# Kernel optimization log

Measured on AMD Instinct MI355X. Metric: run time of the kernel, lower is better.

## Reference

```python
import jax, jax.numpy as jnp
import numpy as np

N = 20000      # nodes
E = 320000     # edges
C = 8          # n_species (input 0e multiplicity)
H = 128        # hidden multiplicity per irrep
RB = 8         # radial basis size
RM = 64        # radial mlp width
CUTOFF = 5.0
P = 2.0        # polynomial cutoff power
AVG_N = 16.0   # avg_n_neighbors
SQRT3 = float(np.sqrt(3.0))


def _w(k, i, o, scale=1.0):
    return jax.random.normal(k, (i, o), jnp.float32) * np.sqrt(scale / i)


def setup_inputs() -> dict:
    key = jax.random.key(0)
    ks = jax.random.split(key, 24)
    return {
        'displacements': jax.random.normal(ks[0], (E, 3), jnp.float32) * 1.5,
        'species': jax.random.randint(ks[1], (N,), 0, C, dtype=jnp.int32),
        'senders': jax.random.randint(ks[2], (E,), 0, N, dtype=jnp.int32),
        'receivers': jax.random.randint(ks[3], (E,), 0, N, dtype=jnp.int32),
        'l1_lin1': _w(ks[4], C, C),
        'l1_rw0': _w(ks[5], RB, RM, 4.0),
        'l1_rw1': _w(ks[6], RM, RM, 4.0),
        'l1_rw2': _w(ks[7], RM, RM, 4.0),
        'l1_rw3': _w(ks[8], RM, 2 * C),
        'l1_w2s': _w(ks[9], C, 2 * H),
        'l1_w2v': _w(ks[10], C, H),
        'l1_skip': jax.random.normal(ks[11], (C, C, 2 * H), jnp.float32) / np.sqrt(C),
        'l2_lin1s': _w(ks[12], H, H),
        'l2_lin1v': _w(ks[13], H, H),
        'l2_rw0': _w(ks[14], RB, RM, 4.0),
        'l2_rw1': _w(ks[15], RM, RM, 4.0),
        'l2_rw2': _w(ks[16], RM, RM, 4.0),
        'l2_rw3': _w(ks[17], RM, 2 * H),
        'l2_w2': _w(ks[18], 2 * H, H),
        'l2_skip': jax.random.normal(ks[19], (C, H, H), jnp.float32) / np.sqrt(H),
        'readout_w': _w(ks[20], H, 1),
    }


def _bessel(x):
    w = jnp.linspace(1.0, RB, RB) * jnp.pi
    xs = x[:, None]
    safe = jnp.where(xs == 0.0, 1.0, xs)
    return (2.0 / CUTOFF) * jnp.where(xs == 0.0, w / CUTOFF, jnp.sin(w * xs / CUTOFF) / safe)


def _poly_cutoff(x):
    u = x / CUTOFF
    out = 1.0 - (P + 1.0) * (P + 2.0) / 2.0 * u ** P \
        + P * (P + 2.0) * u ** (P + 1.0) \
        - P * (P + 1.0) / 2.0 * u ** (P + 2.0)
    return out * jnp.where(u < 1.0, 1.0, 0.0)


def _radial(rb, w0, w1, w2, w3):
    h = jax.nn.silu(rb @ w0)
    h = jax.nn.silu(h @ w1)
    h = jax.nn.silu(h @ w2)
    return h @ w3


def _node_energies(displacements, species, senders, receivers,
                   l1_lin1, l1_rw0, l1_rw1, l1_rw2, l1_rw3, l1_w2s, l1_w2v, l1_skip,
                   l2_lin1s, l2_lin1v, l2_rw0, l2_rw1, l2_rw2, l2_rw3, l2_w2, l2_skip,
                   readout_w):
    sq = jnp.sum(displacements ** 2, axis=-1)
    rn = jnp.where(sq == 0.0, 0.0, jnp.sqrt(jnp.where(sq == 0.0, 1.0, sq)))
    rb = _bessel(rn) * _poly_cutoff(rn)[:, None]                     # (E,RB)
    unit = displacements / jnp.where(rn == 0.0, 1.0, rn)[:, None]
    Y1 = SQRT3 * unit                                                # 1o SH, component norm
    onehot = jax.nn.one_hot(species, C, dtype=displacements.dtype)   # (N,C) = Cx0e features
    inv_sqrt_nbr = 1.0 / np.sqrt(AVG_N)

    # ---- layer 1: Cx0e -> 128x0e + 128x1o ----
    s = (onehot @ l1_lin1)[senders]                                  # (E,C)
    R = _radial(rb, l1_rw0, l1_rw1, l1_rw2, l1_rw3)                  # (E,2C)
    msg_s = s * R[:, :C]                                             # 0e x 0e -> 0e
    msg_v = s[:, :, None] * Y1[:, None, :] * R[:, C:, None]          # 0e x 1o -> 1o (E,C,3)
    agg_s = jax.ops.segment_sum(msg_s, receivers, num_segments=N) * inv_sqrt_nbr
    agg_v = jax.ops.segment_sum(msg_v, receivers, num_segments=N) * inv_sqrt_nbr
    scal = agg_s @ l1_w2s + jnp.einsum('nc,ncd->nd', onehot, l1_skip[species])  # (N,2H)
    vec = jnp.einsum('nci,cd->ndi', agg_v, l1_w2v)                   # (N,H,3)
    # gate: first H even scalars -> silu, last H scalars gate the 1o vectors
    x0 = jax.nn.silu(scal[:, :H])
    x1 = vec * jax.nn.silu(scal[:, H:])[:, :, None]

    # ---- layer 2: 128x0e + 128x1o -> 128x0e ----
    s2 = (x0 @ l2_lin1s)[senders]                                    # (E,H)
    v2 = jnp.einsum('nci,cd->ndi', x1, l2_lin1v)[senders]            # (E,H,3)
    tp = jnp.concatenate([s2, jnp.einsum('eci,ei->ec', v2, Y1) / SQRT3], axis=-1)  # (E,2H)
    R2 = _radial(rb, l2_rw0, l2_rw1, l2_rw2, l2_rw3)                 # (E,2H)
    agg2 = jax.ops.segment_sum(tp * R2, receivers, num_segments=N) * inv_sqrt_nbr
    feat = jax.nn.silu(agg2 @ l2_w2 + jnp.einsum('nc,ncd->nd', x0, l2_skip[species]))

    return feat @ readout_w                                          # (N,1) node energies


def reference(displacements, l1_lin1, l1_rw0, l1_rw1, l1_rw2, l1_rw3, l1_w2s, l1_w2v,
              l1_skip, l2_lin1s, l2_lin1v, l2_rw0, l2_rw1, l2_rw2, l2_rw3, l2_w2,
              l2_skip, readout_w, species, senders, receivers):
    return _node_energies(displacements, species, senders, receivers,
                          l1_lin1, l1_rw0, l1_rw1, l1_rw2, l1_rw3, l1_w2s, l1_w2v, l1_skip,
                          l2_lin1s, l2_lin1v, l2_rw0, l2_rw1, l2_rw2, l2_rw3, l2_w2, l2_skip,
                          readout_w)
```

## Files before the change

kernel.cpp:

```cpp
#include <hip/hip_runtime.h>
#include <math.h>

#define NN_ 20000
#define EE_ 320000

__device__ __forceinline__ float silu_f(float x) { return x / (1.0f + expf(-x)); }

template<int IN, int OUT, bool ACT>
__device__ __forceinline__ void dense(const float* __restrict__ W,
                                      const float* __restrict__ in,
                                      float* __restrict__ out) {
  float acc[OUT];
#pragma unroll
  for (int j = 0; j < OUT; ++j) acc[j] = 0.f;
#pragma unroll
  for (int k = 0; k < IN; ++k) {
    const float x = in[k];
#pragma unroll
    for (int j = 0; j < OUT; ++j) acc[j] = fmaf(x, W[k * OUT + j], acc[j]);
  }
#pragma unroll
  for (int j = 0; j < OUT; ++j) out[j] = ACT ? silu_f(acc[j]) : acc[j];
}

__global__ __launch_bounds__(256) void k_hist(const int* __restrict__ receivers,
                                              int* __restrict__ hist) {
  const int e = blockIdx.x * 256 + threadIdx.x;
  atomicAdd(&hist[receivers[e]], 1);
}

__global__ __launch_bounds__(1024) void k_scan(const int* __restrict__ hist,
                                               int* __restrict__ offs,
                                               int* __restrict__ cursor) {
  __shared__ int lds[1024];
  __shared__ int carry_s;
  const int t = threadIdx.x;
  if (t == 0) carry_s = 0;
  __syncthreads();
  for (int base = 0; base < NN_; base += 1024) {
    const int i = base + t;
    const int v = (i < NN_) ? hist[i] : 0;
    lds[t] = v;
    __syncthreads();
    for (int d = 1; d < 1024; d <<= 1) {
      const int tv = (t >= d) ? lds[t - d] : 0;
      __syncthreads();
      lds[t] += tv;
      __syncthreads();
    }
    const int inc = lds[t];
    const int c = carry_s;
    if (i < NN_) {
      const int off = c + inc - v;
      offs[i] = off;
      cursor[i] = off;
    }
    __syncthreads();
    if (t == 0) carry_s = c + lds[1023];
    __syncthreads();
  }
  if (t == 0) offs[NN_] = carry_s;
}

__global__ __launch_bounds__(256) void k_scatter(const int* __restrict__ receivers,
                                                 int* __restrict__ cursor,
                                                 int* __restrict__ edge_id) {
  const int e = blockIdx.x * 256 + threadIdx.x;
  const int r = receivers[e];
  const int pos = atomicAdd(&cursor[r], 1);
  edge_id[pos] = e;
}

__global__ __launch_bounds__(256) void k1a_edge(
    const float* __restrict__ disp, const int* __restrict__ species,
    const int* __restrict__ senders,
    const float* __restrict__ lin1,
    const float* __restrict__ rw0, const float* __restrict__ rw1,
    const float* __restrict__ rw2, const float* __restrict__ rw3,
    float* __restrict__ buf1, float* __restrict__ rbc_g, float* __restrict__ y1_g) {
  const int e = blockIdx.x * 256 + threadIdx.x;
  const float dx = disp[e * 3 + 0], dy = disp[e * 3 + 1], dz = disp[e * 3 + 2];
  const float sq = dx * dx + dy * dy + dz * dz;
  const float rn = sqrtf(sq);
  const float inv = (rn == 0.f) ? 1.f : (1.f / rn);
  const float u = rn * 0.2f;
  float fc;
  {
    const float u2 = u * u;
    fc = 1.f - 6.f * u2 + 8.f * u2 * u - 3.f * u2 * u2;
    fc = (u < 1.f) ? fc : 0.f;
  }
  float rb[8];
#pragma unroll
  for (int k = 0; k < 8; ++k) {
    const float wk = (float)(k + 1) * 3.14159265358979323846f;
    const float s = (rn == 0.f) ? (wk * 0.2f) : (sinf(wk * u) * inv);
    rb[k] = 0.4f * s * fc;
  }
  float4 r0 = {rb[0], rb[1], rb[2], rb[3]};
  float4 r1 = {rb[4], rb[5], rb[6], rb[7]};
  *(float4*)(rbc_g + e * 8) = r0;
  *(float4*)(rbc_g + e * 8 + 4) = r1;
  const float y1x = 1.7320508075688772f * dx * inv;
  const float y1y = 1.7320508075688772f * dy * inv;
  const float y1z = 1.7320508075688772f * dz * inv;
  float4 y4 = {y1x, y1y, y1z, 0.f};
  *(float4*)(y1_g + e * 4) = y4;

  float h0[64], h1[64], R[16];
  dense<8, 64, true>(rw0, rb, h0);
  dense<64, 64, true>(rw1, h0, h1);
  dense<64, 64, true>(rw2, h1, h0);
  dense<64, 16, false>(rw3, h0, R);

  const int sp = species[senders[e]];
  float m[32];
#pragma unroll
  for (int c = 0; c < 8; ++c) {
    const float sc = lin1[sp * 8 + c];
    m[c] = sc * R[c];
    const float mv = sc * R[8 + c];
    m[8 + c * 3 + 0] = mv * y1x;
    m[8 + c * 3 + 1] = mv * y1y;
    m[8 + c * 3 + 2] = mv * y1z;
  }
  float* dst = buf1 + (size_t)e * 32;
#pragma unroll
  for (int q = 0; q < 8; ++q) {
    float4 v = {m[q * 4 + 0], m[q * 4 + 1], m[q * 4 + 2], m[q * 4 + 3]};
    *(float4*)(dst + q * 4) = v;
  }
}

__global__ __launch_bounds__(256) void k1b_gather(
    const float* __restrict__ buf1, const int* __restrict__ offs,
    const int* __restrict__ edge_id,
    float* __restrict__ agg_s, float* __restrict__ agg_v) {
  const int n = blockIdx.x * 8 + (threadIdx.x >> 5);
  const int ch = threadIdx.x & 31;
  const int beg = offs[n], end = offs[n + 1];
  float acc = 0.f;
  for (int i = beg; i < end; ++i) {
    const int eid = edge_id[i];
    acc += buf1[(size_t)eid * 32 + ch];
  }
  if (ch < 8) agg_s[n * 8 + ch] = acc;
  else agg_v[n * 24 + (ch - 8)] = acc;
}

__global__ __launch_bounds__(64) void k2a_node(
    const float* __restrict__ agg_s, const float* __restrict__ agg_v,
    const int* __restrict__ species,
    const float* __restrict__ w2s, const float* __restrict__ w2v,
    const float* __restrict__ skip1,
    float* __restrict__ x0_g, float* __restrict__ x1_g) {
  const int n = blockIdx.x;
  const int l = threadIdx.x;
  __shared__ float g_lds[128];
  const int sp = species[n];
  float as[8];
#pragma unroll
  for (int k = 0; k < 8; ++k) as[k] = agg_s[n * 8 + k] * 0.25f;
  float sc[4];
#pragma unroll
  for (int j = 0; j < 4; ++j) {
    const int d = l * 4 + j;
    float a = skip1[(sp * 9) * 256 + d];
#pragma unroll
    for (int k = 0; k < 8; ++k) a = fmaf(as[k], w2s[k * 256 + d], a);
    sc[j] = silu_f(a);
  }
  if (l < 32) {
#pragma unroll
    for (int j = 0; j < 4; ++j) x0_g[n * 128 + l * 4 + j] = sc[j];
  } else {
#pragma unroll
    for (int j = 0; j < 4; ++j) g_lds[(l - 32) * 4 + j] = sc[j];
  }
  __syncthreads();
  float av[24];
#pragma unroll
  for (int k = 0; k < 24; ++k) av[k] = agg_v[n * 24 + k] * 0.25f;
#pragma unroll
  for (int h = 0; h < 2; ++h) {
    const int d = l + h * 64;
    const float g = g_lds[d];
    float v0 = 0.f, v1 = 0.f, v2v = 0.f;
#pragma unroll
    for (int c = 0; c < 8; ++c) {
      const float w = w2v[c * 128 + d];
      v0 = fmaf(av[c * 3 + 0], w, v0);
      v1 = fmaf(av[c * 3 + 1], w, v1);
      v2v = fmaf(av[c * 3 + 2], w, v2v);
    }
    x1_g[(n * 3 + 0) * 128 + d] = v0 * g;
    x1_g[(n * 3 + 1) * 128 + d] = v1 * g;
    x1_g[(n * 3 + 2) * 128 + d] = v2v * g;
  }
}

__global__ __launch_bounds__(256) void k2b_gemm(
    const float* __restrict__ x0_g, const float* __restrict__ x1_g,
    const int* __restrict__ species,
    const float* __restrict__ lin1s, const float* __restrict__ lin1v,
    const float* __restrict__ skip2,
    float* __restrict__ s2_g, float* __restrict__ v2_g,
    float* __restrict__ skipv_g) {
  const int w = __builtin_amdgcn_readfirstlane((int)(threadIdx.x >> 6));
  const int l = threadIdx.x & 63;
  const int nbase = blockIdx.x * 32 + w * 8;
  float s2a[8] = {}, s2b[8] = {}, ska[8] = {}, skb[8] = {};
  float v2a[8][3] = {}, v2b[8][3] = {};
  int sp[8];
#pragma unroll
  for (int nn = 0; nn < 8; ++nn) sp[nn] = species[nbase + nn];
  for (int c = 0; c < 128; ++c) {
    const float wA0 = lin1s[c * 128 + l];
    const float wA1 = lin1s[c * 128 + 64 + l];
    const float wB0 = lin1v[c * 128 + l];
    const float wB1 = lin1v[c * 128 + 64 + l];
#pragma unroll
    for (int nn = 0; nn < 8; ++nn) {
      const int n = nbase + nn;
      const float x0v = x0_g[n * 128 + c];
      const float wS0 = skip2[sp[nn] * 16384 + c * 128 + l];
      const float wS1 = skip2[sp[nn] * 16384 + c * 128 + 64 + l];
      s2a[nn] = fmaf(x0v, wA0, s2a[nn]);
      s2b[nn] = fmaf(x0v, wA1, s2b[nn]);
      ska[nn] = fmaf(x0v, wS0, ska[nn]);
      skb[nn] = fmaf(x0v, wS1, skb[nn]);
#pragma unroll
      for (int i = 0; i < 3; ++i) {
        const float x1v = x1_g[(n * 3 + i) * 128 + c];
        v2a[nn][i] = fmaf(x1v, wB0, v2a[nn][i]);
        v2b[nn][i] = fmaf(x1v, wB1, v2b[nn][i]);
      }
    }
  }
#pragma unroll
  for (int nn = 0; nn < 8; ++nn) {
    const int n = nbase + nn;
    s2_g[n * 128 + l] = s2a[nn];
    s2_g[n * 128 + 64 + l] = s2b[nn];
    skipv_g[n * 128 + l] = ska[nn];
    skipv_g[n * 128 + 64 + l] = skb[nn];
#pragma unroll
    for (int i = 0; i < 3; ++i) {
      v2_g[n * 384 + l * 3 + i] = v2a[nn][i];
      v2_g[n * 384 + (64 + l) * 3 + i] = v2b[nn][i];
    }
  }
}

__global__ __launch_bounds__(256) void k3a_edge(
    const float* __restrict__ rbc_g,
    const float* __restrict__ rw0, const float* __restrict__ rw1,
    const float* __restrict__ rw2,
    float* __restrict__ ha_buf) {
  const int e = blockIdx.x * 256 + threadIdx.x;
  float rb[8];
  {
    const float4 a = *(const float4*)(rbc_g + e * 8);
    const float4 b = *(const float4*)(rbc_g + e * 8 + 4);
    rb[0] = a.x; rb[1] = a.y; rb[2] = a.z; rb[3] = a.w;
    rb[4] = b.x; rb[5] = b.y; rb[6] = b.z; rb[7] = b.w;
  }
  float h0[64], h1[64];
  dense<8, 64, true>(rw0, rb, h0);
  dense<64, 64, true>(rw1, h0, h1);
  dense<64, 64, true>(rw2, h1, h0);
  float* dst = ha_buf + (size_t)e * 64;
#pragma unroll
  for (int q = 0; q < 16; ++q) {
    float4 v = {h0[q * 4 + 0], h0[q * 4 + 1], h0[q * 4 + 2], h0[q * 4 + 3]};
    *(float4*)(dst + q * 4) = v;
  }
}

__global__ __launch_bounds__(256) void k3b_gather(
    const float* __restrict__ ha_buf, const float* __restrict__ y1_g,
    const int* __restrict__ senders,
    const int* __restrict__ offs, const int* __restrict__ edge_id,
    const float* __restrict__ rw3,
    const float* __restrict__ s2_g, const float* __restrict__ v2_g,
    float* __restrict__ agg2) {
  const int n = blockIdx.x;
  const int ch = threadIdx.x;
  float w[64];
#pragma unroll
  for (int k = 0; k < 64; ++k) w[k] = rw3[k * 256 + ch];
  const int beg = offs[n], end = offs[n + 1];
  const bool is_s = ch < 128;
  const int c3 = (ch - 128) * 3;
  float acc = 0.f;
  for (int i = beg; i < end; ++i) {
    const int eid = __builtin_amdgcn_readfirstlane(edge_id[i]);
    const int s = __builtin_amdgcn_readfirstlane(senders[eid]);
    const float y1x = y1_g[eid * 4 + 0];
    const float y1y = y1_g[eid * 4 + 1];
    const float y1z = y1_g[eid * 4 + 2];
    float tp;
    if (is_s) {
      tp = s2_g[(size_t)s * 128 + ch];
    } else {
      tp = (v2_g[(size_t)s * 384 + c3 + 0] * y1x +
            v2_g[(size_t)s * 384 + c3 + 1] * y1y +
            v2_g[(size_t)s * 384 + c3 + 2] * y1z) * 0.5773502691896258f;
    }
    const float* ha = ha_buf + (size_t)eid * 64;
    float r0 = 0.f, r1 = 0.f, r2 = 0.f, r3 = 0.f;
#pragma unroll
    for (int k = 0; k < 64; k += 4) {
      r0 = fmaf(ha[k + 0], w[k + 0], r0);
      r1 = fmaf(ha[k + 1], w[k + 1], r1);
      r2 = fmaf(ha[k + 2], w[k + 2], r2);
      r3 = fmaf(ha[k + 3], w[k + 3], r3);
    }
    acc = fmaf(tp, (r0 + r1) + (r2 + r3), acc);
  }
  agg2[(size_t)n * 256 + ch] = acc;
}

__global__ __launch_bounds__(256) void k4_node(
    const float* __restrict__ agg2, const float* __restrict__ skipv,
    const float* __restrict__ w2, const float* __restrict__ readout,
    float* __restrict__ out) {
  __shared__ float tile[64 * 65];
  __shared__ float partial[256];
  const int t = threadIdx.x;
  const int w = __builtin_amdgcn_readfirstlane((int)(threadIdx.x >> 6));
  const int l = t & 63;
  const int n0 = blockIdx.x * 64;
  const int n = n0 + l;
  float acc[32];
#pragma unroll
  for (int j = 0; j < 32; ++j) acc[j] = 0.f;
  for (int ko = 0; ko < 256; ko += 64) {
    __syncthreads();
#pragma unroll
    for (int rep = 0; rep < 16; ++rep) {
      const int lin = rep * 256 + t;
      const int node = lin >> 6, kk = lin & 63;
      const int gn = n0 + node;
      tile[kk * 65 + node] = (gn < NN_) ? agg2[(size_t)gn * 256 + ko + kk] * 0.25f : 0.f;
    }
    __syncthreads();
    for (int kk = 0; kk < 64; ++kk) {
      const float a = tile[kk * 65 + l];
#pragma unroll
      for (int jj = 0; jj < 32; ++jj)
        acc[jj] = fmaf(a, w2[(ko + kk) * 128 + w * 32 + jj], acc[jj]);
    }
  }
  float po = 0.f;
  if (n < NN_) {
#pragma unroll
    for (int jj = 0; jj < 32; ++jj) {
      const int d = w * 32 + jj;
      const float v = acc[jj] + skipv[n * 128 + d];
      po = fmaf(silu_f(v), readout[d], po);
    }
  }
  partial[w * 64 + l] = po;
  __syncthreads();
  if (t < 64 && n0 + t < NN_) {
    out[n0 + t] = partial[t] + partial[64 + t] + partial[128 + t] + partial[192 + t];
  }
}

extern "C" void kernel_launch(void* const* d_in, const int* in_sizes, int n_in,
                              void* d_out, int out_size, void* d_ws, size_t ws_size,
                              hipStream_t stream) {
  const float* disp = (const float*)d_in[0];
  const int* species = (const int*)d_in[1];
  const int* senders = (const int*)d_in[2];
  const int* receivers = (const int*)d_in[3];
  const float* l1_lin1 = (const float*)d_in[4];
  const float* l1_rw0 = (const float*)d_in[5];
  const float* l1_rw1 = (const float*)d_in[6];
  const float* l1_rw2 = (const float*)d_in[7];
  const float* l1_rw3 = (const float*)d_in[8];
  const float* l1_w2s = (const float*)d_in[9];
  const float* l1_w2v = (const float*)d_in[10];
  const float* l1_skip = (const float*)d_in[11];
  const float* l2_lin1s = (const float*)d_in[12];
  const float* l2_lin1v = (const float*)d_in[13];
  const float* l2_rw0 = (const float*)d_in[14];
  const float* l2_rw1 = (const float*)d_in[15];
  const float* l2_rw2 = (const float*)d_in[16];
  const float* l2_rw3 = (const float*)d_in[17];
  const float* l2_w2 = (const float*)d_in[18];
  const float* l2_skip = (const float*)d_in[19];
  const float* readout_w = (const float*)d_in[20];

  float* ws = (float*)d_ws;
  float* rbc   = ws;
  float* y1    = ws + 2560000;
  float* s2    = ws + 3840000;
  float* v2    = ws + 6400000;
  float* skipv = ws + 14080000;
  float* agg2  = ws + 16640000;
  float* pool  = ws + 21760000;
  float* agg_s = pool;
  float* agg_v = pool + 160000;
  float* buf1  = pool + 640000;
  float* x0    = pool + 640000;
  float* x1    = pool + 3200000;
  float* ha    = pool;
  int* ibase   = (int*)(ws + 42240000);
  int* hist    = ibase;
  int* cursor  = ibase + 20000;
  int* offs    = ibase + 40000;
  int* edge_id = ibase + 60001;
  if (ws_size < (size_t)(42240000 + 380001) * 4) return;

  hipMemsetAsync(hist, 0, 20000 * sizeof(int), stream);
  k_hist<<<EE_ / 256, 256, 0, stream>>>(receivers, hist);
  k_scan<<<1, 1024, 0, stream>>>(hist, offs, cursor);
  k_scatter<<<EE_ / 256, 256, 0, stream>>>(receivers, cursor, edge_id);

  k1a_edge<<<EE_ / 256, 256, 0, stream>>>(disp, species, senders, l1_lin1,
                                          l1_rw0, l1_rw1, l1_rw2, l1_rw3,
                                          buf1, rbc, y1);
  k1b_gather<<<NN_ / 8, 256, 0, stream>>>(buf1, offs, edge_id, agg_s, agg_v);
  k2a_node<<<NN_, 64, 0, stream>>>(agg_s, agg_v, species, l1_w2s, l1_w2v, l1_skip,
                                   x0, x1);
  k2b_gemm<<<NN_ / 32, 256, 0, stream>>>(x0, x1, species, l2_lin1s, l2_lin1v,
                                         l2_skip, s2, v2, skipv);

  k3a_edge<<<EE_ / 256, 256, 0, stream>>>(rbc, l2_rw0, l2_rw1, l2_rw2, ha);
  k3b_gather<<<NN_, 256, 0, stream>>>(ha, y1, senders, offs, edge_id, l2_rw3,
                                      s2, v2, agg2);
  k4_node<<<(NN_ + 63) / 64, 256, 0, stream>>>(agg2, skipv, l2_w2, readout_w,
                                               (float*)d_out);
}
```

Measured before the change: 1.310 ms.

## Tile radial MLP layers through shared memory with register-blocked 8x8 outer products

The per-edge radial MLP in both layers is changed from one thread per edge holding 64-wide hidden vectors in registers, with weights read from global memory, to a block-cooperative scheme. Each block stages 128 edges' activations and one layer's weights in LDS and computes an 8-edge by 8-output register tile per thread. The aim is to cut register pressure and spilling and to reuse weights across edges. In exchange it adds several block barriers per layer and roughly 50KB of LDS per block, which limits occupancy. The last 64-to-16 layer in layer 1 still reads its weights from global memory per thread.

```diff
diff --git a/kernel.cpp b/kernel.cpp
--- a/kernel.cpp
+++ b/kernel.cpp
@@ -3,24 +3,62 @@
 
 #define NN_ 20000
 #define EE_ 320000
+#define SHP 68
 
 __device__ __forceinline__ float silu_f(float x) { return x / (1.0f + expf(-x)); }
 
-template<int IN, int OUT, bool ACT>
-__device__ __forceinline__ void dense(const float* __restrict__ W,
-                                      const float* __restrict__ in,
-                                      float* __restrict__ out) {
-  float acc[OUT];
-#pragma unroll
-  for (int j = 0; j < OUT; ++j) acc[j] = 0.f;
-#pragma unroll
-  for (int k = 0; k < IN; ++k) {
-    const float x = in[k];
-#pragma unroll
-    for (int j = 0; j < OUT; ++j) acc[j] = fmaf(x, W[k * OUT + j], acc[j]);
-  }
-#pragma unroll
-  for (int j = 0; j < OUT; ++j) out[j] = ACT ? silu_f(acc[j]) : acc[j];
+template<int KD>
+__device__ __forceinline__ void layer_step(float* __restrict__ sh_h,
+                                           const float* __restrict__ sh_w,
+                                           int wavebase, int eg, int jg) {
+  const int jb = jg * 8;
+  float acc[8][8];
+#pragma unroll
+  for (int ee = 0; ee < 8; ++ee)
+#pragma unroll
+    for (int jj = 0; jj < 8; ++jj) acc[ee][jj] = 0.f;
+
+#pragma unroll
+  for (int kc = 0; kc < KD; kc += 4) {
+    float4 w4[4][2];
+#pragma unroll
+    for (int kk = 0; kk < 4; ++kk) {
+      w4[kk][0] = *(const float4*)&sh_w[(kc + kk) * 64 + jb];
+      w4[kk][1] = *(const float4*)&sh_w[(kc + kk) * 64 + jb + 4];
+    }
+    float4 h4[8];
+#pragma unroll
+    for (int ee = 0; ee < 8; ++ee)
+      h4[ee] = *(const float4*)&sh_h[(wavebase + eg + 8 * ee) * SHP + kc];
+#pragma unroll
+    for (int kk = 0; kk < 4; ++kk) {
+#pragma unroll
+      for (int ee = 0; ee < 8; ++ee) {
+        const float hv = ((const float*)&h4[ee])[kk];
+        acc[ee][0] = fmaf(hv, w4[kk][0].x, acc[ee][0]);
+        acc[ee][1] = fmaf(hv, w4[kk][0].y, acc[ee][1]);
+        acc[ee][2] = fmaf(hv, w4[kk][0].z, acc[ee][2]);
+        acc[ee][3] = fmaf(hv, w4[kk][0].w, acc[ee][3]);
+        acc[ee][4] = fmaf(hv, w4[kk][1].x, acc[ee][4]);
+        acc[ee][5] = fmaf(hv, w4[kk][1].y, acc[ee][5]);
+        acc[ee][6] = fmaf(hv, w4[kk][1].z, acc[ee][6]);
+        acc[ee][7] = fmaf(hv, w4[kk][1].w, acc[ee][7]);
+      }
+    }
+  }
+#pragma unroll
+  for (int ee = 0; ee < 8; ++ee) {
+    float* dst = &sh_h[(wavebase + eg + 8 * ee) * SHP + jb];
+    float4 lo = {silu_f(acc[ee][0]), silu_f(acc[ee][1]), silu_f(acc[ee][2]), silu_f(acc[ee][3])};
+    float4 hi = {silu_f(acc[ee][4]), silu_f(acc[ee][5]), silu_f(acc[ee][6]), silu_f(acc[ee][7])};
+    *(float4*)dst = lo;
+    *(float4*)(dst + 4) = hi;
+  }
+}
+
+__device__ __forceinline__ void load_w(const float* __restrict__ W, int nfloat,
+                                       float* __restrict__ dst, int t) {
+  for (int i = t * 4; i < nfloat; i += 512) *(float4*)(dst + i) = *(const float4*)(W + i);
 }
 
 __global__ __launch_bounds__(256) void k_hist(const int* __restrict__ receivers,
@@ -71,14 +109,19 @@
   edge_id[pos] = e;
 }
 
-__global__ __launch_bounds__(256) void k1a_edge(
+__global__ __launch_bounds__(128) void k1a_radial(
     const float* __restrict__ disp, const int* __restrict__ species,
     const int* __restrict__ senders,
     const float* __restrict__ lin1,
     const float* __restrict__ rw0, const float* __restrict__ rw1,
     const float* __restrict__ rw2, const float* __restrict__ rw3,
     float* __restrict__ buf1, float* __restrict__ rbc_g, float* __restrict__ y1_g) {
-  const int e = blockIdx.x * 256 + threadIdx.x;
+  __shared__ float sh_h[128 * SHP];
+  __shared__ float sh_w[64 * 64];
+  const int t = threadIdx.x;
+  const int e0 = blockIdx.x * 128;
+  const int e = e0 + t;
+
   const float dx = disp[e * 3 + 0], dy = disp[e * 3 + 1], dz = disp[e * 3 + 2];
   const float sq = dx * dx + dy * dy + dz * dz;
   const float rn = sqrtf(sq);
@@ -106,12 +149,34 @@
   const float y1z = 1.7320508075688772f * dz * inv;
   float4 y4 = {y1x, y1y, y1z, 0.f};
   *(float4*)(y1_g + e * 4) = y4;
-
-  float h0[64], h1[64], R[16];
-  dense<8, 64, true>(rw0, rb, h0);
-  dense<64, 64, true>(rw1, h0, h1);
-  dense<64, 64, true>(rw2, h1, h0);
-  dense<64, 16, false>(rw3, h0, R);
+  *(float4*)&sh_h[t * SHP] = r0;
+  *(float4*)&sh_h[t * SHP + 4] = r1;
+
+  const int wavebase = (t >> 6) * 64;
+  const int lane = t & 63;
+  const int eg = lane >> 3, jg = lane & 7;
+
+  load_w(rw0, 8 * 64, sh_w, t);
+  __syncthreads();
+  layer_step<8>(sh_h, sh_w, wavebase, eg, jg);
+  __syncthreads();
+  load_w(rw1, 64 * 64, sh_w, t);
+  __syncthreads();
+  layer_step<64>(sh_h, sh_w, wavebase, eg, jg);
+  __syncthreads();
+  load_w(rw2, 64 * 64, sh_w, t);
+  __syncthreads();
+  layer_step<64>(sh_h, sh_w, wavebase, eg, jg);
+  __syncthreads();
+
+  float R[16];
+#pragma unroll
+  for (int c = 0; c < 16; ++c) R[c] = 0.f;
+  for (int k = 0; k < 64; ++k) {
+    const float h = sh_h[t * SHP + k];
+#pragma unroll
+    for (int c = 0; c < 16; ++c) R[c] = fmaf(h, rw3[k * 16 + c], R[c]);
+  }
 
   const int sp = species[senders[e]];
   float m[32];
@@ -129,6 +194,45 @@
   for (int q = 0; q < 8; ++q) {
     float4 v = {m[q * 4 + 0], m[q * 4 + 1], m[q * 4 + 2], m[q * 4 + 3]};
     *(float4*)(dst + q * 4) = v;
+  }
+}
+
+__global__ __launch_bounds__(128) void k3a_radial(
+    const float* __restrict__ rbc_g,
+    const float* __restrict__ rw0, const float* __restrict__ rw1,
+    const float* __restrict__ rw2,
+    float* __restrict__ ha_buf) {
+  __shared__ float sh_h[128 * SHP];
+  __shared__ float sh_w[64 * 64];
+  const int t = threadIdx.x;
+  const int e0 = blockIdx.x * 128;
+
+  *(float4*)&sh_h[t * SHP] = *(const float4*)(rbc_g + (size_t)(e0 + t) * 8);
+  *(float4*)&sh_h[t * SHP + 4] = *(const float4*)(rbc_g + (size_t)(e0 + t) * 8 + 4);
+
+  const int wavebase = (t >> 6) * 64;
+  const int lane = t & 63;
+  const int eg = lane >> 3, jg = lane & 7;
+
+  load_w(rw0, 8 * 64, sh_w, t);
+  __syncthreads();
+  layer_step<8>(sh_h, sh_w, wavebase, eg, jg);
+  __syncthreads();
+  load_w(rw1, 64 * 64, sh_w, t);
+  __syncthreads();
+  layer_step<64>(sh_h, sh_w, wavebase, eg, jg);
+  __syncthreads();
+  load_w(rw2, 64 * 64, sh_w, t);
+  __syncthreads();
+  layer_step<64>(sh_h, sh_w, wavebase, eg, jg);
+  __syncthreads();
+
+#pragma unroll
+  for (int r = 0; r < 16; ++r) {
+    const int lin = r * 128 + t;
+    const int el = lin >> 4;
+    const int k = (lin & 15) * 4;
+    *(float4*)(ha_buf + (size_t)(e0 + el) * 64 + k) = *(const float4*)&sh_h[el * SHP + k];
   }
 }
 
@@ -249,31 +353,6 @@
       v2_g[n * 384 + l * 3 + i] = v2a[nn][i];
       v2_g[n * 384 + (64 + l) * 3 + i] = v2b[nn][i];
     }
-  }
-}
-
-__global__ __launch_bounds__(256) void k3a_edge(
-    const float* __restrict__ rbc_g,
-    const float* __restrict__ rw0, const float* __restrict__ rw1,
-    const float* __restrict__ rw2,
-    float* __restrict__ ha_buf) {
-  const int e = blockIdx.x * 256 + threadIdx.x;
-  float rb[8];
-  {
-    const float4 a = *(const float4*)(rbc_g + e * 8);
-    const float4 b = *(const float4*)(rbc_g + e * 8 + 4);
-    rb[0] = a.x; rb[1] = a.y; rb[2] = a.z; rb[3] = a.w;
-    rb[4] = b.x; rb[5] = b.y; rb[6] = b.z; rb[7] = b.w;
-  }
-  float h0[64], h1[64];
-  dense<8, 64, true>(rw0, rb, h0);
-  dense<64, 64, true>(rw1, h0, h1);
-  dense<64, 64, true>(rw2, h1, h0);
-  float* dst = ha_buf + (size_t)e * 64;
-#pragma unroll
-  for (int q = 0; q < 16; ++q) {
-    float4 v = {h0[q * 4 + 0], h0[q * 4 + 1], h0[q * 4 + 2], h0[q * 4 + 3]};
-    *(float4*)(dst + q * 4) = v;
   }
 }
 
@@ -419,16 +498,16 @@
   k_scan<<<1, 1024, 0, stream>>>(hist, offs, cursor);
   k_scatter<<<EE_ / 256, 256, 0, stream>>>(receivers, cursor, edge_id);
 
-  k1a_edge<<<EE_ / 256, 256, 0, stream>>>(disp, species, senders, l1_lin1,
-                                          l1_rw0, l1_rw1, l1_rw2, l1_rw3,
-                                          buf1, rbc, y1);
+  k1a_radial<<<EE_ / 128, 128, 0, stream>>>(disp, species, senders, l1_lin1,
+                                            l1_rw0, l1_rw1, l1_rw2, l1_rw3,
+                                            buf1, rbc, y1);
   k1b_gather<<<NN_ / 8, 256, 0, stream>>>(buf1, offs, edge_id, agg_s, agg_v);
   k2a_node<<<NN_, 64, 0, stream>>>(agg_s, agg_v, species, l1_w2s, l1_w2v, l1_skip,
                                    x0, x1);
   k2b_gemm<<<NN_ / 32, 256, 0, stream>>>(x0, x1, species, l2_lin1s, l2_lin1v,
                                          l2_skip, s2, v2, skipv);
 
-  k3a_edge<<<EE_ / 256, 256, 0, stream>>>(rbc, l2_rw0, l2_rw1, l2_rw2, ha);
+  k3a_radial<<<EE_ / 128, 128, 0, stream>>>(rbc, l2_rw0, l2_rw1, l2_rw2, ha);
   k3b_gather<<<NN_, 256, 0, stream>>>(ha, y1, senders, offs, edge_id, l2_rw3,
                                       s2, v2, agg2);
   k4_node<<<(NN_ + 63) / 64, 256, 0, stream>>>(agg2, skipv, l2_w2, readout_w,
```

New measurement: 1.092 ms. 1.2x faster.
